# Kernel optimization log

Measured on AMD Instinct MI355X. Metric: run time of the kernel, lower is better.

## Reference

```python
import jax, jax.numpy as jnp
import numpy as np

CODEBOOK_SIZE = 8192
TOKEN_SIZE = 256
COMMITMENT_COST = 0.25
B, C, H, W = 32, 256, 32, 32


def setup_inputs() -> dict:
    key = jax.random.key(0)
    k1, k2 = jax.random.split(key)
    z = jax.random.normal(k1, (B, C, H, W), dtype=jnp.float32)
    # torch init: uniform_(-1/codebook_size, 1/codebook_size)
    embedding = jax.random.uniform(
        k2, (CODEBOOK_SIZE, TOKEN_SIZE), dtype=jnp.float32,
        minval=-1.0 / CODEBOOK_SIZE, maxval=1.0 / CODEBOOK_SIZE)
    return {"z": z, "embedding": embedding}


def reference(z, embedding):
    # b c h w -> b h w c
    z = jnp.transpose(z.astype(jnp.float32), (0, 2, 3, 1))
    b, h, w, c = z.shape
    z_flat = z.reshape(-1, c)  # [N, c]

    # squared euclidean distances: ||z||^2 + ||e||^2 - 2 z e^T
    d = (jnp.sum(z_flat ** 2, axis=1, keepdims=True)
         + jnp.sum(embedding ** 2, axis=1)
         - 2.0 * jnp.einsum('nd,kd->nk', z_flat, embedding))  # [N, K]
    idx = jnp.argmin(d, axis=1)  # [N]

    z_q = embedding[idx].reshape(z.shape)  # [b,h,w,c]

    commitment_loss = COMMITMENT_COST * jnp.mean(
        (jax.lax.stop_gradient(z_q) - z) ** 2)
    codebook_loss = jnp.mean((z_q - jax.lax.stop_gradient(z)) ** 2)
    loss = commitment_loss + codebook_loss

    # straight-through estimator
    z_q_st = z + jax.lax.stop_gradient(z_q - z)
    z_q_out = jnp.transpose(z_q_st, (0, 3, 1, 2))  # b h w c -> b c h w

    min_encoding_indices = idx.reshape(b, h, w)
    return (z_q_out, loss, commitment_loss, codebook_loss,
            min_encoding_indices)
```

## Files before the change

kernel.cpp:

```cpp
#include <hip/hip_runtime.h>
#include <float.h>

#define NBATCH 32
#define NCHAN  256
#define NHW    1024
#define NTOK   32768
#define NK     8192
#define ND     256
#define ZELEMS 8388608
#define OUT_LOSS 8388608
#define OUT_IDX  8388611
#define MARGIN   1.2e-4f

typedef short bf16x8  __attribute__((ext_vector_type(8)));
typedef float f32x4   __attribute__((ext_vector_type(4)));
typedef float f32x16  __attribute__((ext_vector_type(16)));

__device__ __forceinline__ unsigned short f2bf(float f) {
    unsigned int u = __float_as_uint(f);
    u += 0x7FFFu + ((u >> 16) & 1u);
    return (unsigned short)(u >> 16);
}

__device__ __forceinline__ float embed8(float x, int code) {
    return __int_as_float((__float_as_int(x) & 0xFFFFFF00) | code);
}


__global__ __launch_bounds__(256) void k_cast(const float* __restrict__ zg,
                                              const float* __restrict__ E,
                                              unsigned short* __restrict__ Epre,
                                              unsigned short* __restrict__ Zpre,
                                              float* __restrict__ en,
                                              float* __restrict__ acc,
                                              int* __restrict__ counter) {
    __shared__ unsigned short buf[128][34];
    const int t = threadIdx.x;
    if (blockIdx.x < 1024) {
        int g = blockIdx.x * 256 + t;
        int code = g >> 5, c16 = g & 31;
        int kc = c16 >> 2, ks = (c16 >> 1) & 1, lhi = c16 & 1;
        const float4* E4 = (const float4*)(E + code * ND + c16 * 8);
        float4 a = E4[0], b = E4[1];
        float s = a.x*a.x + a.y*a.y + a.z*a.z + a.w*a.w
                + b.x*b.x + b.y*b.y + b.z*b.z + b.w*b.w;
        #pragma unroll
        for (int off = 1; off < 32; off <<= 1) s += __shfl_xor(s, off, 64);
        if ((t & 31) == 0) en[code] = s;
        unsigned int u[4];
        u[0] = (unsigned int)f2bf(a.x) | ((unsigned int)f2bf(a.y) << 16);
        u[1] = (unsigned int)f2bf(a.z) | ((unsigned int)f2bf(a.w) << 16);
        u[2] = (unsigned int)f2bf(b.x) | ((unsigned int)f2bf(b.y) << 16);
        u[3] = (unsigned int)f2bf(b.z) | ((unsigned int)f2bf(b.w) << 16);
        *(uint4*)((char*)Epre + (size_t)(code >> 7) * 65536 + kc * 8192
                  + (ks * 2 + lhi) * 2048 + (code & 127) * 16) =
            make_uint4(u[0], u[1], u[2], u[3]);
        if (blockIdx.x == 0 && t == 0) { acc[0] = 0.0f; counter[0] = 0; }
    } else {
        int bi = blockIdx.x - 1024;
        int b = bi >> 6, kc = (bi >> 3) & 7, hwt = bi & 7;
        int c0 = kc * 32, hw0 = hwt * 128;
        #pragma unroll
        for (int r = 0; r < 4; ++r) {
            int idx = r * 256 + t;
            int c = idx >> 5, q = idx & 31;
            float4 v = *(const float4*)&zg[(b * 256 + c0 + c) * 1024 + hw0 + q * 4];
            buf[q * 4 + 0][c] = f2bf(v.x);
            buf[q * 4 + 1][c] = f2bf(v.y);
            buf[q * 4 + 2][c] = f2bf(v.z);
            buf[q * 4 + 3][c] = f2bf(v.w);
        }
        __syncthreads();
        int tok = t >> 1, ks = t & 1;
        char* base = (char*)Zpre + (size_t)((b * 8 + hwt) * 8 + kc) * 8192;
        #pragma unroll
        for (int lhi = 0; lhi < 2; ++lhi) {
            unsigned int u[4];
            #pragma unroll
            for (int k = 0; k < 4; ++k) {
                int cc = ks * 16 + lhi * 8 + 2 * k;
                u[k] = (unsigned int)buf[tok][cc] | ((unsigned int)buf[tok][cc + 1] << 16);
            }
            *(uint4*)(base + (ks * 2 + lhi) * 2048 + tok * 16) =
                make_uint4(u[0], u[1], u[2], u[3]);
        }
    }
}

__global__ __launch_bounds__(256, 2) void k_dist(const unsigned short* __restrict__ Epre,
                                                 const unsigned short* __restrict__ Zpre,
                                                 const float* __restrict__ en,
                                                 float2* __restrict__ part2) {
    __shared__ __align__(16) char Elds[3][16384];
    __shared__ float2 red[2][128];
    __shared__ float en_s[256];

    const int t    = threadIdx.x;
    const int kbb2 = blockIdx.x;
    const int mb   = blockIdx.y;
    const int n0   = mb * 128;
    const int w    = t >> 6, lane = t & 63;
    const int l31  = lane & 31, lhi = lane >> 5;
    const int wm   = w >> 1, wn = w & 1;

    const char* Esrc = (const char*)Epre + (size_t)kbb2 * 131072;
    const char* Zsrc = (const char*)Zpre + (size_t)mb * 65536;

    auto STAGE_E = [&](int bb, int kc) {
        #pragma unroll
        for (int s2 = 0; s2 < 2; ++s2)
            #pragma unroll
            for (int h = 0; h < 2; ++h)
                __builtin_amdgcn_global_load_lds(
                    (const unsigned int*)(Esrc + (size_t)s2 * 65536 + kc * 8192 + h * 4096 + t * 16),
                    (unsigned int*)&Elds[bb][s2 * 8192 + h * 4096 + t * 16], 16, 0, 0);
    };

    bf16x8 zbR[2][2][2];
    const char* Zp = Zsrc + lhi * 2048 + (wn * 64 + l31) * 16;
    auto LOADZ = [&](int set, int kc) {
        const char* p = Zp + kc * 8192;
        #pragma unroll
        for (int j = 0; j < 2; ++j)
            #pragma unroll
            for (int ks = 0; ks < 2; ++ks)
                zbR[set][j][ks] = *(const bf16x8*)(p + ks * 4096 + j * 512);
    };

    f32x16 acc[4][2];
    #pragma unroll
    for (int i = 0; i < 4; ++i)
        #pragma unroll
        for (int j = 0; j < 2; ++j) acc[i][j] = (f32x16)0.0f;

    STAGE_E(0, 0);
    STAGE_E(1, 1);
    LOADZ(0, 0);
    en_s[t] = en[kbb2 * 256 + t];
    __syncthreads();

    #pragma unroll
    for (int kc = 0; kc < 8; ++kc) {
        const int pp = kc & 1, eb = kc % 3;
        if (kc == 1 || kc == 7) {
            asm volatile("s_waitcnt vmcnt(8)" ::: "memory");
            __builtin_amdgcn_s_barrier();
        } else if (kc >= 2) {
            asm volatile("s_waitcnt vmcnt(12)" ::: "memory");
            __builtin_amdgcn_s_barrier();
        }
        if (kc < 6) STAGE_E((kc + 2) % 3, kc + 2);
        if (kc < 7) LOADZ(pp ^ 1, kc + 1);

        const char* Eb = &Elds[eb][0] + wm * 8192 + lhi * 2048 + l31 * 16;
        bf16x8 ea[4][2];
        #pragma unroll
        for (int i = 0; i < 4; ++i)
            #pragma unroll
            for (int ks = 0; ks < 2; ++ks)
                ea[i][ks] = *(const bf16x8*)(Eb + ks * 4096 + i * 512);

        __builtin_amdgcn_s_setprio(1);
        #pragma unroll
        for (int ks = 0; ks < 2; ++ks)
            #pragma unroll
            for (int i = 0; i < 4; ++i)
                #pragma unroll
                for (int j = 0; j < 2; ++j)
                    acc[i][j] = __builtin_amdgcn_mfma_f32_32x32x16_bf16(
                        ea[i][ks], zbR[pp][j][ks], acc[i][j], 0, 0, 0);
        __builtin_amdgcn_s_setprio(0);
    }

    __syncthreads();

    float v1[2][4], v2[2][4];
    #pragma unroll
    for (int j = 0; j < 2; ++j)
        #pragma unroll
        for (int i = 0; i < 4; ++i) { v1[j][i] = FLT_MAX; v2[j][i] = FLT_MAX; }
    #pragma unroll
    for (int i = 0; i < 4; ++i) {
        const int cb = wm * 128 + i * 32 + lhi * 4;
        #pragma unroll
        for (int rq = 0; rq < 4; ++rq) {
            f32x4 ev = *(const f32x4*)&en_s[cb + 8 * rq];
            #pragma unroll
            for (int rr = 0; rr < 4; ++rr) {
                const int r = rq * 4 + rr;
                const int code = cb + 8 * rq + rr;
                #pragma unroll
                for (int j = 0; j < 2; ++j) {
                    float s  = fmaf(-2.0f, acc[i][j][r], ev[rr]);
                    float se = embed8(s, code);
                    v2[j][i] = __builtin_amdgcn_fmed3f(se, v1[j][i], v2[j][i]);
                    v1[j][i] = fminf(v1[j][i], se);
                }
            }
        }
    }
    float m1[2], m2[2];
    #pragma unroll
    for (int j = 0; j < 2; ++j) {
        float a1 = fminf(v1[j][0], v1[j][1]);
        float ah = fmaxf(v1[j][0], v1[j][1]);
        float a2 = fminf(ah, fminf(v2[j][0], v2[j][1]));
        float b1 = fminf(v1[j][2], v1[j][3]);
        float bh = fmaxf(v1[j][2], v1[j][3]);
        float b2 = fminf(bh, fminf(v2[j][2], v2[j][3]));
        m1[j] = fminf(a1, b1);
        m2[j] = fminf(fmaxf(a1, b1), fminf(a2, b2));
    }
    #pragma unroll
    for (int j = 0; j < 2; ++j) {
        float b1 = __shfl_xor(m1[j], 32, 64);
        float b2 = __shfl_xor(m2[j], 32, 64);
        float hi = fmaxf(m1[j], b1);
        m1[j] = fminf(m1[j], b1);
        m2[j] = fminf(fminf(hi, m2[j]), b2);
    }
    if (lane < 32) {
        #pragma unroll
        for (int j = 0; j < 2; ++j)
            red[wm][wn * 64 + j * 32 + l31] = make_float2(m1[j], m2[j]);
    }
    __syncthreads();
    if (t < 128) {
        float2 A = red[0][t], B = red[1][t];
        float g1 = fminf(A.x, B.x);
        float g2 = fminf(fminf(fmaxf(A.x, B.x), A.y), B.y);
        part2[(size_t)kbb2 * NTOK + n0 + t] = make_float2(g1, g2);
    }
}

__global__ __launch_bounds__(256) void k_refine(const float* __restrict__ zg,
                                                const float* __restrict__ E,
                                                const float2* __restrict__ part2,
                                                int* __restrict__ idxw,
                                                float* __restrict__ outF) {
    __shared__ float Zs[256 * 65];
    const int t = threadIdx.x;
    const int n0 = blockIdx.x * 64;
    const int b = n0 >> 10, hw0 = n0 & 1023;

    #pragma unroll
    for (int r = 0; r < 16; ++r) {
        int li = r * 256 + t;
        int c = li >> 4, q = li & 15;
        float4 v = *(const float4*)&zg[(b * 256 + c) * 1024 + hw0 + q * 4];
        Zs[c * 65 + q * 4 + 0] = v.x;
        Zs[c * 65 + q * 4 + 1] = v.y;
        Zs[c * 65 + q * 4 + 2] = v.z;
        Zs[c * 65 + q * 4 + 3] = v.w;
    }
    __syncthreads();

    const int w = t >> 6, l = t & 63;
    for (int it = 0; it < 16; ++it) {
        const int tokl = w * 16 + it;
        const int n = n0 + tokl;

        float zreg[4];
        #pragma unroll
        for (int j = 0; j < 4; ++j) zreg[j] = Zs[(64 * j + l) * 65 + tokl];

        double z2 = 0.0;
        #pragma unroll
        for (int j = 0; j < 4; ++j) z2 += (double)zreg[j] * (double)zreg[j];
        #pragma unroll
        for (int m = 1; m < 64; m <<= 1) z2 += __shfl_xor(z2, m, 64);
        const float z2f = (float)z2;

        float2 p = make_float2(FLT_MAX, FLT_MAX);
        if (l < 32) p = part2[(size_t)l * NTOK + n];
        int code1 = (l << 8) | (__float_as_int(p.x) & 0xFF);
        int code2 = (l << 8) | (__float_as_int(p.y) & 0xFF);

        float vmin = p.x;
        #pragma unroll
        for (int m = 1; m < 64; m <<= 1) vmin = fminf(vmin, __shfl_xor(vmin, m, 64));
        const float thr = vmin + MARGIN;

        unsigned long long m1 = __ballot(p.x <= thr);
        unsigned long long m2 = __ballot(p.y <= thr);

        float bdq = FLT_MAX; int bidx = 0x7fffffff;
        #pragma unroll
        for (int pass = 0; pass < 2; ++pass) {
            unsigned long long mm = pass ? m2 : m1;
            int ibits = pass ? code2 : code1;
            while (mm) {
                int src = __ffsll(mm) - 1; mm &= mm - 1;
                int cidx = __shfl(ibits, src, 64);
                const float* erow = E + cidx * ND;
                double g = (double)zreg[0] * (double)erow[l]
                         + (double)zreg[1] * (double)erow[64 + l]
                         + (double)zreg[2] * (double)erow[128 + l]
                         + (double)zreg[3] * (double)erow[192 + l];
                #pragma unroll
                for (int mk = 1; mk < 64; mk <<= 1) g += __shfl_xor(g, mk, 64);
                float c  = (float)(2.0 * g);
                float dq = z2f - c;
                if (dq < bdq || (dq == bdq && cidx < bidx)) { bdq = dq; bidx = cidx; }
            }
        }
        if (l == 0) { idxw[n] = bidx; outF[OUT_IDX + n] = (float)bidx; }
    }
}

__global__ __launch_bounds__(256) void k_gather(const float* __restrict__ E,
                                                const float* __restrict__ zg,
                                                const int* __restrict__ idxw,
                                                float* __restrict__ out,
                                                float* __restrict__ acc,
                                                int* __restrict__ counter) {
    __shared__ __align__(16) float Es[64 * 256];
    __shared__ int sidx[64];
    __shared__ float wred[4];
    const int t = threadIdx.x;
    const int b = blockIdx.x >> 4, ht = blockIdx.x & 15;

    if (t < 64) sidx[t] = idxw[b * 1024 + ht * 64 + t];
    __syncthreads();
    const float4* E4 = (const float4*)E;
    #pragma unroll
    for (int r = 0; r < 16; ++r) {
        int li = r * 256 + t;
        int row = li >> 6, slot = li & 63;
        float4 v = E4[(size_t)sidx[row] * 64 + slot];
        *(float4*)&Es[row * 256 + ((slot ^ (row & 15)) * 4)] = v;
    }
    __syncthreads();

    const int hw = t & 63, wv = t >> 6;
    float s = 0.0f;
    #pragma unroll 8
    for (int cc = 0; cc < 64; ++cc) {
        int c = wv * 64 + cc;
        float e = Es[hw * 256 + (((c >> 2) ^ (hw & 15)) * 4) + (c & 3)];
        size_t gi = (size_t)(b * 256 + c) * 1024 + ht * 64 + hw;
        float zv = zg[gi];
        out[gi] = e;
        float d = e - zv;
        s = fmaf(d, d, s);
    }
    #pragma unroll
    for (int off = 32; off > 0; off >>= 1) s += __shfl_down(s, off, 64);
    if ((t & 63) == 0) wred[wv] = s;
    __syncthreads();
    if (t == 0) {
        atomicAdd(acc, wred[0] + wred[1] + wred[2] + wred[3]);
        __threadfence();
        int old = atomicAdd(counter, 1);
        if (old == 511) {
            float total = atomicAdd(acc, 0.0f);
            float mse = total / 8388608.0f;
            out[OUT_LOSS + 0] = 1.25f * mse;
            out[OUT_LOSS + 1] = 0.25f * mse;
            out[OUT_LOSS + 2] = mse;
        }
    }
}

extern "C" void kernel_launch(void* const* d_in, const int* in_sizes, int n_in,
                              void* d_out, int out_size, void* d_ws, size_t ws_size,
                              hipStream_t stream) {
    const float* zg = (const float*)d_in[0];
    const float* E  = (const float*)d_in[1];
    float* out = (float*)d_out;
    float* wsf = (float*)d_ws;
    float*  acc     = wsf;
    int*    counter = (int*)(wsf + 1);
    float*  en      = wsf + 64;
    int*    idxw    = (int*)(wsf + 64 + NK);
    float2* part2   = (float2*)(wsf + 64 + NK + NTOK);
    unsigned short* Epre = (unsigned short*)(wsf + 64 + NK + NTOK + 4194304);
    unsigned short* Zpre = (unsigned short*)d_out;

    k_cast  <<<3072, 256, 0, stream>>>(zg, E, Epre, Zpre, en, acc, counter);
    k_dist  <<<dim3(32, 256), 256, 0, stream>>>(Epre, Zpre, en, part2);
    k_refine<<<NTOK / 64, 256, 0, stream>>>(zg, E, part2, idxw, out);
    k_gather<<<512, 256, 0, stream>>>(E, zg, idxw, out, acc, counter);
}
```

Before: 299.9 us.

## Stage Z tiles through LDS and compute loss from refine distances

The distance kernel now stages the Z operand into a triple-buffered LDS ring with async global-to-LDS loads, alongside E, instead of keeping register double buffers loaded from global memory. The per-stage wait/barrier schedule is restructured around this ring. The loss is now computed in the refine kernel from the exact distance (||e||^2 - 2g + ||z||^2) accumulated in double. This removes the z re-read and reduction from the gather kernel. The trade-off is more LDS per block (possible occupancy pressure), plus an extra barrier per iteration.

```diff
diff --git a/kernel.cpp b/kernel.cpp
--- a/kernel.cpp
+++ b/kernel.cpp
@@ -32,7 +32,7 @@
                                               unsigned short* __restrict__ Epre,
                                               unsigned short* __restrict__ Zpre,
                                               float* __restrict__ en,
-                                              float* __restrict__ acc,
+                                              double* __restrict__ acc,
                                               int* __restrict__ counter) {
     __shared__ unsigned short buf[128][34];
     const int t = threadIdx.x;
@@ -55,7 +55,7 @@
         *(uint4*)((char*)Epre + (size_t)(code >> 7) * 65536 + kc * 8192
                   + (ks * 2 + lhi) * 2048 + (code & 127) * 16) =
             make_uint4(u[0], u[1], u[2], u[3]);
-        if (blockIdx.x == 0 && t == 0) { acc[0] = 0.0f; counter[0] = 0; }
+        if (blockIdx.x == 0 && t == 0) { acc[0] = 0.0; counter[0] = 0; }
     } else {
         int bi = blockIdx.x - 1024;
         int b = bi >> 6, kc = (bi >> 3) & 7, hwt = bi & 7;
@@ -92,6 +92,7 @@
                                                  const float* __restrict__ en,
                                                  float2* __restrict__ part2) {
     __shared__ __align__(16) char Elds[3][16384];
+    __shared__ __align__(16) char Zlds[3][8192];
     __shared__ float2 red[2][128];
     __shared__ float en_s[256];
 
@@ -106,7 +107,7 @@
     const char* Esrc = (const char*)Epre + (size_t)kbb2 * 131072;
     const char* Zsrc = (const char*)Zpre + (size_t)mb * 65536;
 
-    auto STAGE_E = [&](int bb, int kc) {
+    auto STAGE = [&](int bb, int kc) {
         #pragma unroll
         for (int s2 = 0; s2 < 2; ++s2)
             #pragma unroll
@@ -114,51 +115,48 @@
                 __builtin_amdgcn_global_load_lds(
                     (const unsigned int*)(Esrc + (size_t)s2 * 65536 + kc * 8192 + h * 4096 + t * 16),
                     (unsigned int*)&Elds[bb][s2 * 8192 + h * 4096 + t * 16], 16, 0, 0);
+        #pragma unroll
+        for (int h = 0; h < 2; ++h)
+            __builtin_amdgcn_global_load_lds(
+                (const unsigned int*)(Zsrc + kc * 8192 + h * 4096 + t * 16),
+                (unsigned int*)&Zlds[bb][h * 4096 + t * 16], 16, 0, 0);
     };
 
-    bf16x8 zbR[2][2][2];
-    const char* Zp = Zsrc + lhi * 2048 + (wn * 64 + l31) * 16;
-    auto LOADZ = [&](int set, int kc) {
-        const char* p = Zp + kc * 8192;
-        #pragma unroll
-        for (int j = 0; j < 2; ++j)
-            #pragma unroll
-            for (int ks = 0; ks < 2; ++ks)
-                zbR[set][j][ks] = *(const bf16x8*)(p + ks * 4096 + j * 512);
-    };
-
     f32x16 acc[4][2];
     #pragma unroll
     for (int i = 0; i < 4; ++i)
         #pragma unroll
         for (int j = 0; j < 2; ++j) acc[i][j] = (f32x16)0.0f;
 
-    STAGE_E(0, 0);
-    STAGE_E(1, 1);
-    LOADZ(0, 0);
-    en_s[t] = en[kbb2 * 256 + t];
-    __syncthreads();
+    float en_v = en[kbb2 * 256 + t];
+    STAGE(0, 0);
+    STAGE(1, 1);
+    asm volatile("s_waitcnt vmcnt(6)" ::: "memory");
+    __builtin_amdgcn_s_barrier();
+
+    const int eoff = wm * 8192 + lhi * 2048 + l31 * 16;
+    const int zoff = lhi * 2048 + (wn * 64 + l31) * 16;
 
     #pragma unroll
     for (int kc = 0; kc < 8; ++kc) {
-        const int pp = kc & 1, eb = kc % 3;
-        if (kc == 1 || kc == 7) {
-            asm volatile("s_waitcnt vmcnt(8)" ::: "memory");
-            __builtin_amdgcn_s_barrier();
-        } else if (kc >= 2) {
-            asm volatile("s_waitcnt vmcnt(12)" ::: "memory");
-            __builtin_amdgcn_s_barrier();
-        }
-        if (kc < 6) STAGE_E((kc + 2) % 3, kc + 2);
-        if (kc < 7) LOADZ(pp ^ 1, kc + 1);
-
-        const char* Eb = &Elds[eb][0] + wm * 8192 + lhi * 2048 + l31 * 16;
-        bf16x8 ea[4][2];
+        const int pp = kc % 3;
+        const char* Eb = &Elds[pp][0] + eoff;
+        const char* Zb = &Zlds[pp][0] + zoff;
+        bf16x8 ea[4][2], zb[2][2];
         #pragma unroll
         for (int i = 0; i < 4; ++i)
             #pragma unroll
             for (int ks = 0; ks < 2; ++ks)
                 ea[i][ks] = *(const bf16x8*)(Eb + ks * 4096 + i * 512);
+        #pragma unroll
+        for (int j = 0; j < 2; ++j)
+            #pragma unroll
+            for (int ks = 0; ks < 2; ++ks)
+                zb[j][ks] = *(const bf16x8*)(Zb + ks * 4096 + j * 512);
+        asm volatile("s_waitcnt lgkmcnt(0)" ::: "memory");
+        __builtin_amdgcn_s_barrier();
+        __builtin_amdgcn_sched_barrier(0);
+        if (kc < 6) STAGE((kc + 2) % 3, kc + 2);
 
         __builtin_amdgcn_s_setprio(1);
         #pragma unroll
@@ -168,10 +166,13 @@
                 #pragma unroll
                 for (int j = 0; j < 2; ++j)
                     acc[i][j] = __builtin_amdgcn_mfma_f32_32x32x16_bf16(
-                        ea[i][ks], zbR[pp][j][ks], acc[i][j], 0, 0, 0);
+                        ea[i][ks], zb[j][ks], acc[i][j], 0, 0, 0);
         __builtin_amdgcn_s_setprio(0);
-    }
-
+        if (kc < 6)      { asm volatile("s_waitcnt vmcnt(6)" ::: "memory"); __builtin_amdgcn_s_barrier(); }
+        else if (kc == 6){ asm volatile("s_waitcnt vmcnt(0)" ::: "memory"); __builtin_amdgcn_s_barrier(); }
+    }
+
+    en_s[t] = en_v;
     __syncthreads();
 
     float v1[2][4], v2[2][4];
@@ -235,10 +236,14 @@
 
 __global__ __launch_bounds__(256) void k_refine(const float* __restrict__ zg,
                                                 const float* __restrict__ E,
+                                                const float* __restrict__ en,
                                                 const float2* __restrict__ part2,
                                                 int* __restrict__ idxw,
-                                                float* __restrict__ outF) {
+                                                float* __restrict__ outF,
+                                                double* __restrict__ acc,
+                                                int* __restrict__ counter) {
     __shared__ float Zs[256 * 65];
+    __shared__ double lred[4];
     const int t = threadIdx.x;
     const int n0 = blockIdx.x * 64;
     const int b = n0 >> 10, hw0 = n0 & 1023;
@@ -256,6 +261,7 @@
     __syncthreads();
 
     const int w = t >> 6, l = t & 63;
+    double lsum = 0.0;
     for (int it = 0; it < 16; ++it) {
         const int tokl = w * 16 + it;
         const int n = n0 + tokl;
@@ -284,7 +290,7 @@
         unsigned long long m1 = __ballot(p.x <= thr);
         unsigned long long m2 = __ballot(p.y <= thr);
 
-        float bdq = FLT_MAX; int bidx = 0x7fffffff;
+        float bdq = FLT_MAX; int bidx = 0x7fffffff; double gw = 0.0;
         #pragma unroll
         for (int pass = 0; pass < 2; ++pass) {
             unsigned long long mm = pass ? m2 : m1;
@@ -301,22 +307,35 @@
                 for (int mk = 1; mk < 64; mk <<= 1) g += __shfl_xor(g, mk, 64);
                 float c  = (float)(2.0 * g);
                 float dq = z2f - c;
-                if (dq < bdq || (dq == bdq && cidx < bidx)) { bdq = dq; bidx = cidx; }
+                if (dq < bdq || (dq == bdq && cidx < bidx)) { bdq = dq; bidx = cidx; gw = g; }
             }
         }
-        if (l == 0) { idxw[n] = bidx; outF[OUT_IDX + n] = (float)bidx; }
+        if (l == 0) {
+            idxw[n] = bidx; outF[OUT_IDX + n] = (float)bidx;
+            lsum += (double)en[bidx] - 2.0 * gw + z2;
+        }
+    }
+    if (l == 0) lred[w] = lsum;
+    __syncthreads();
+    if (t == 0) {
+        atomicAdd(acc, lred[0] + lred[1] + lred[2] + lred[3]);
+        __threadfence();
+        int old = atomicAdd(counter, 1);
+        if (old == 511) {
+            double total = atomicAdd(acc, 0.0);
+            double mse = total / 8388608.0;
+            outF[OUT_LOSS + 0] = (float)(1.25 * mse);
+            outF[OUT_LOSS + 1] = (float)(0.25 * mse);
+            outF[OUT_LOSS + 2] = (float)mse;
+        }
     }
 }
 
 __global__ __launch_bounds__(256) void k_gather(const float* __restrict__ E,
-                                                const float* __restrict__ zg,
                                                 const int* __restrict__ idxw,
-                                                float* __restrict__ out,
-                                                float* __restrict__ acc,
-                                                int* __restrict__ counter) {
+                                                float* __restrict__ out) {
     __shared__ __align__(16) float Es[64 * 256];
     __shared__ int sidx[64];
-    __shared__ float wred[4];
     const int t = threadIdx.x;
     const int b = blockIdx.x >> 4, ht = blockIdx.x & 15;
 
@@ -333,32 +352,12 @@
     __syncthreads();
 
     const int hw = t & 63, wv = t >> 6;
-    float s = 0.0f;
     #pragma unroll 8
     for (int cc = 0; cc < 64; ++cc) {
         int c = wv * 64 + cc;
         float e = Es[hw * 256 + (((c >> 2) ^ (hw & 15)) * 4) + (c & 3)];
         size_t gi = (size_t)(b * 256 + c) * 1024 + ht * 64 + hw;
-        float zv = zg[gi];
         out[gi] = e;
-        float d = e - zv;
-        s = fmaf(d, d, s);
-    }
-    #pragma unroll
-    for (int off = 32; off > 0; off >>= 1) s += __shfl_down(s, off, 64);
-    if ((t & 63) == 0) wred[wv] = s;
-    __syncthreads();
-    if (t == 0) {
-        atomicAdd(acc, wred[0] + wred[1] + wred[2] + wred[3]);
-        __threadfence();
-        int old = atomicAdd(counter, 1);
-        if (old == 511) {
-            float total = atomicAdd(acc, 0.0f);
-            float mse = total / 8388608.0f;
-            out[OUT_LOSS + 0] = 1.25f * mse;
-            out[OUT_LOSS + 1] = 0.25f * mse;
-            out[OUT_LOSS + 2] = mse;
-        }
     }
 }
 
@@ -369,8 +368,8 @@
     const float* E  = (const float*)d_in[1];
     float* out = (float*)d_out;
     float* wsf = (float*)d_ws;
-    float*  acc     = wsf;
-    int*    counter = (int*)(wsf + 1);
+    double* acc     = (double*)wsf;
+    int*    counter = (int*)(wsf + 2);
     float*  en      = wsf + 64;
     int*    idxw    = (int*)(wsf + 64 + NK);
     float2* part2   = (float2*)(wsf + 64 + NK + NTOK);
@@ -379,6 +378,6 @@
 
     k_cast  <<<3072, 256, 0, stream>>>(zg, E, Epre, Zpre, en, acc, counter);
     k_dist  <<<dim3(32, 256), 256, 0, stream>>>(Epre, Zpre, en, part2);
-    k_refine<<<NTOK / 64, 256, 0, stream>>>(zg, E, part2, idxw, out);
-    k_gather<<<512, 256, 0, stream>>>(E, zg, idxw, out, acc, counter);
-}
+    k_refine<<<NTOK / 64, 256, 0, stream>>>(zg, E, en, part2, idxw, out, acc, counter);
+    k_gather<<<512, 256, 0, stream>>>(E, idxw, out);
+}
```

After: 282.1 us. -6.0%, faster.
